# Kernel optimization log

Measured on AMD Instinct MI355X. Metric: run time of the kernel, lower is better.

The kernel has to match this reference:

```python
import jax, jax.numpy as jnp
from jax import lax
import numpy as np

R_ICO = 6          # resolution exponent r
CIN, COUT = 64, 64
RIN, ROUT = 6, 6
CHARTS = 5
H, W = 2 ** R_ICO, 2 ** (R_ICO + 1)
BATCH = 4


def _build_reorder_idx(r, R):
    H_, W_ = 2 ** r, 2 ** (r + 1)
    p = 2 ** r
    idx_in = np.arange(R * 5 * H_ * W_, dtype=np.int64).reshape(R, 5, H_, W_)
    out = np.zeros((R, 5, H_ + 2, W_ + 2), dtype=np.int64)
    out[..., 1:-1, 1:-1] = idx_in
    out[..., 0, 1:p + 1] = np.roll(idx_in, 1, -3)[..., -1, p:]
    out[..., 0, p + 1:-1] = np.roll(np.roll(idx_in, 1, -3), -1, -4)[..., :, -1][..., ::-1]
    out[..., -1, 2:p + 2] = np.roll(np.roll(idx_in, -1, -3), -1, -4)[..., :, 0][..., ::-1]
    out[..., -1, p + 1:-1] = np.roll(idx_in, -1, -3)[..., 0, 0:p]
    out[..., 1:-1, 0] = np.roll(np.roll(idx_in, 1, -3), 1, -4)[..., -1, 0:p][..., ::-1]
    out[..., 2:, -1] = np.roll(np.roll(idx_in, -1, -3), 1, -4)[..., 0, p:][..., ::-1]
    return out


_REORDER = jnp.asarray(_build_reorder_idx(R_ICO, RIN))

# 'baseline' hexagonal kernel index table (idx_k2 == idx_k for baseline)
_IDX_K = np.array([
    [5, 4, -1, 6, 0, 3, -1, 1, 2],
    [4, 3, -1, 5, 0, 2, -1, 6, 1],
    [3, 2, -1, 4, 0, 1, -1, 5, 6],
    [2, 1, -1, 3, 0, 6, -1, 4, 5],
    [1, 6, -1, 2, 0, 5, -1, 3, 4],
    [6, 5, -1, 1, 0, 4, -1, 2, 3]], dtype=np.int64) % 7
# per-output-rotation roll of the Rin axis: idx_r = arange(Rin) rolled i times
_RIN_MAP = np.stack([np.roll(np.arange(RIN), i) for i in range(ROUT)])  # (Rout, Rin)
_MASK3 = np.ones((3, 3), dtype=np.float32)
_MASK3[0, 2] = 0.0  # ret[..., 0, 2] = 0
_MASK3[2, 0] = 0.0  # ret[..., 2, 0] = 0

# CleanVertices: zero the two pole vertices of each chart
_VMASK = np.ones((H, W), dtype=np.float32)
_VMASK[0, -1] = 0.0
_VMASK[-1, 0] = 0.0


def _expand_kernel(weight):
    # weight: (Cout, Cin, Rin, 7)
    # K[co, ci, i, rj, k] = weight[co, ci, rin_map[i, rj], idx_k[i, k]]
    K = weight[:, :, _RIN_MAP[:, :, None], _IDX_K[:, None, :]]  # (Cout, Cin, Rout, Rin, 9)
    K = K.transpose(0, 2, 1, 3, 4).reshape(COUT, ROUT, CIN, RIN, 3, 3)
    K = K * _MASK3  # zero hex-grid corner taps
    # kernel_type='baseline' => idx_k2 == idx_k, so 0.5*K + 0.5*K2 == K
    return K.reshape(COUT * ROUT, CIN * RIN, 3, 3)


def setup_inputs() -> dict:
    key = jax.random.key(0)
    kx, kw = jax.random.split(key)
    s = float(np.sqrt(2.0 / (3 * 3 * CIN * RIN)))
    x = jax.random.normal(kx, (BATCH, CIN, RIN, CHARTS, H, W), dtype=jnp.float32)
    weight = s * jax.random.normal(kw, (COUT, CIN, RIN, 7), dtype=jnp.float32)
    bias = jnp.zeros((COUT,), dtype=jnp.float32)
    return {"x": x, "weight": weight, "bias": bias}


def reference(x, weight, bias):
    B = x.shape[0]
    # CleanVertices on input (inside PadIco.process_vertices)
    x = x * _VMASK
    # icosahedral gather padding: [B, C, R, 5, H, W] -> [B, C, R, 5, H+2, W+2]
    xf = x.reshape(B, CIN, -1)
    xp = jnp.take(xf, _REORDER, axis=-1)
    # fold (C R) -> channels and (charts, H+2) -> height
    ximg = xp.reshape(B, CIN * RIN, CHARTS * (H + 2), W + 2)
    kernel = _expand_kernel(weight)
    y = lax.conv_general_dilated(ximg, kernel, (1, 1), ((1, 1), (1, 1)),
                                 dimension_numbers=('NCHW', 'OIHW', 'NCHW'))
    y = y + jnp.repeat(bias, ROUT)[None, :, None, None]
    y = y.reshape(B, COUT, ROUT, CHARTS, H + 2, W + 2)[..., 1:-1, 1:-1]
    # CleanVertices on output
    return y * _VMASK
```

## Files before the change

### kernel.cpp

```cpp
#include <hip/hip_runtime.h>
#include <hip/hip_bf16.h>

#define BB    4
#define CIN_  64
#define RIN_  6
#define CH_   5
#define HH    64
#define WW_   128
#define KD    384
#define MD    384
#define PH    66
#define PW    130
#define PSZ   (PH*PW)

#define NTAP 7
#define WEXP2_ELEMS (NTAP*MD*KD)
#define WEXP2_BYTES (WEXP2_ELEMS*2)
#define NBORD 388

typedef __hip_bfloat16 bf16;
typedef __attribute__((ext_vector_type(8))) short bf16x8;
typedef __attribute__((ext_vector_type(4))) float f32x4;

__device__ const int TMAP[NTAP] = {0,1,3,4,5,7,8};
__device__ const int IDXK[6][9] = {
    {5,4,6,6,0,3,6,1,2},
    {4,3,6,5,0,2,6,6,1},
    {3,2,6,4,0,1,6,5,6},
    {2,1,6,3,0,6,6,4,5},
    {1,6,6,2,0,5,6,3,4},
    {6,5,6,1,0,4,6,2,3},
};

__global__ void wexp2_kernel(const float* __restrict__ w, bf16* __restrict__ W2) {
    int e = blockIdx.x * blockDim.x + threadIdx.x;
    if (e >= WEXP2_ELEMS) return;
    int k  = e % KD;
    int m  = (e / KD) % MD;
    int tt = e / (KD * MD);
    int t  = TMAP[tt];
    int co = m / 6, ro = m % 6, ci = k / 6, ri = k % 6;
    int rw = (ri - ro + 6) % 6;
    int s  = IDXK[ro][t];
    W2[e] = __float2bfloat16(w[((co * CIN_ + ci) * RIN_ + rw) * 7 + s]);
}

__global__ __launch_bounds__(256) void pad_interior(const float* __restrict__ x,
                                                    bf16* __restrict__ P) {
    int bid  = blockIdx.x;
    int kblk = bid % 3;
    int xh   = (bid / 3) & 1;
    int y    = (bid / 6) % 64;
    int bc   = bid / 384;
    int c = bc % 5, b = bc / 5;

    int lane = threadIdx.x & 63;
    int wv   = threadIdx.x >> 6;
    int k0   = kblk * 128 + wv * 32;
    int sx   = xh * 64 + lane;
    int xx   = sx + 1;

    bool mask0 = (y == 0 && sx == 127) || (y == 63 && sx == 0);

    const float* src = x + ((((size_t)(b * 384 + k0) * 5 + c) * 64 + y) * 128 + sx);
    unsigned int hbuf[16];
    #pragma unroll
    for (int kk = 0; kk < 32; kk += 2) {
        float v1 = src[(size_t)kk * 40960];
        float v2 = src[(size_t)(kk + 1) * 40960];
        if (mask0) { v1 = 0.f; v2 = 0.f; }
        bf16 h1 = __float2bfloat16(v1);
        bf16 h2 = __float2bfloat16(v2);
        hbuf[kk >> 1] = ((unsigned int)*(unsigned short*)&h2 << 16) |
                        (unsigned int)*(unsigned short*)&h1;
    }
    bf16* dst = P + (((size_t)(b * 5 + c) * PH + (y + 1)) * PW + xx) * KD + k0;
    uint4* d4 = (uint4*)dst;
    #pragma unroll
    for (int q = 0; q < 4; ++q)
        d4[q] = make_uint4(hbuf[4*q], hbuf[4*q+1], hbuf[4*q+2], hbuf[4*q+3]);
}

__global__ void pad_border(const float* __restrict__ x, bf16* __restrict__ P) {
    int e = blockIdx.x * blockDim.x + threadIdx.x;
    if (e >= 20 * NBORD * KD) return;
    int k  = e % KD;
    int p  = (e / KD) % NBORD;
    int bc = e / (KD * NBORD);
    int c = bc % 5, b = bc / 5;
    int yy, xx;
    if (p < 130)      { yy = 0;  xx = p; }
    else if (p < 260) { yy = 65; xx = p - 130; }
    else if (p < 324) { yy = 1 + (p - 260); xx = 0; }
    else              { yy = 1 + (p - 324); xx = 129; }

    int ci = k / RIN_, r = k % RIN_;
    int sr = r, sc = c, sy = 0, sx = 0;
    bool zi = false;
    if (xx == 129) {
        if (yy >= 2) { sr = (r + 5) % 6; sc = (c + 1) % 5; sy = 0; sx = 129 - yy; }
        else zi = true;
    } else if (yy == 0) {
        if (xx >= 1 && xx <= 64)        { sc = (c + 4) % 5; sy = 63; sx = 63 + xx; }
        else if (xx >= 65 && xx <= 128) { sr = (r + 1) % 6; sc = (c + 4) % 5; sy = 128 - xx; sx = 127; }
        else zi = true;
    } else if (yy == 65) {
        if (xx >= 65 && xx <= 128)      { sc = (c + 1) % 5; sy = 0; sx = xx - 65; }
        else if (xx >= 2 && xx <= 64)   { sr = (r + 1) % 6; sc = (c + 1) % 5; sy = 65 - xx; sx = 0; }
        else zi = true;
    } else {
        sr = (r + 5) % 6; sc = (c + 4) % 5; sy = 63; sx = 64 - yy;
    }
    if (zi) { sr = 0; sc = 0; sy = 0; sx = 0; }
    float v = x[((((size_t)b * 384 + (ci * 6 + sr)) * 5 + sc) * 64 + sy) * 128 + sx];
    if ((sy == 0 && sx == 127) || (sy == 63 && sx == 0)) v = 0.f;
    P[(((size_t)(b * 5 + c) * PH + yy) * PW + xx) * KD + k] = __float2bfloat16(v);
}

#define DYP 0x2950
#define DXP 0x2644

#define GLD(g, l) __builtin_amdgcn_global_load_lds( \
    (const __attribute__((address_space(1))) void*)(g), \
    (__attribute__((address_space(3))) void*)(l), 16, 0, 0)
#define MFMA_(a, b, c) __builtin_amdgcn_mfma_f32_16x16x32_bf16((a), (b), (c), 0, 0, 0)

__global__ __launch_bounds__(512) void conv_mfma8(
        const bf16* __restrict__ P, const bf16* __restrict__ W2,
        const float* __restrict__ bias, float* __restrict__ out) {
    __shared__ __align__(16) bf16 As[3][4096];
    __shared__ __align__(16) bf16 Bs[3][8192];

    const int bid = blockIdx.x;
    const int w   = (bid & 7) * 240 + (bid >> 3);
    const int mblk  = w % 3;
    const int ntile = (w / 3) % 32;
    const int bc    = w / 96;
    const int c = bc % 5, b = bc / 5;
    const int y0 = ntile * 2;

    const int tid  = threadIdx.x;
    const int lane = tid & 63;
    const int wv   = tid >> 6;
    const int wm   = wv >> 2, wn = wv & 3;
    const int lm   = lane & 15, lg = lane >> 4;

    const bf16* Pslice = P + (size_t)(b * 5 + c) * PSZ * KD;

    const int rA  = tid >> 2;
    const int kg  = (tid & 3) ^ ((rA >> 1) & 3);
    const bf16* gA0 = W2 + (size_t)(mblk * 128 + rA) * KD + kg * 8;
    const bf16* gB0 = Pslice + (size_t)rA * KD + kg * 8;

    int oA[4], oB[4];
    #pragma unroll
    for (int i = 0; i < 4; ++i) {
        int mm = wm * 64 + i * 16 + lm;
        oA[i] = (mm * 4 + (lg ^ ((mm >> 1) & 3))) * 16;
        int nn = wn * 64 + i * 16 + lm;
        oB[i] = (nn * 4 + (lg ^ ((nn >> 1) & 3))) * 16;
    }
    const char* Ab = (const char*)&As[0][0];
    const char* Bb = (const char*)&Bs[0][0];

    f32x4 acc[4][4] = {};

    #pragma unroll
    for (int t = 0; t < 2; ++t) {
        const bf16* ga = gA0 + t * 32;
        const bf16* gb = gB0 + (size_t)y0 * PW * KD + t * 32;
        GLD(ga, &As[t][wv * 512]);
        GLD(gb, &Bs[t][wv * 512]);
        GLD(gb + (size_t)PW * KD, &Bs[t][4096 + wv * 512]);
    }
    asm volatile("s_waitcnt vmcnt(3)" ::: "memory");
    __builtin_amdgcn_s_barrier();

    #pragma unroll 1
    for (int tt = 0; tt < 7; ++tt) {
        #pragma unroll
        for (int kc = 0; kc < 12; ++kc) {
            const int rb   = kc % 3;
            const int sb   = (kc + 2) % 3;
            const int skc  = (kc + 2) % 12;
            const int stt  = tt + (kc + 2) / 12;
            const bool dostage = (stt < 7);

            bf16x8 a0 = *(const bf16x8*)(Ab + rb * 8192 + oA[0]);
            bf16x8 a1 = *(const bf16x8*)(Ab + rb * 8192 + oA[1]);
            bf16x8 a2 = *(const bf16x8*)(Ab + rb * 8192 + oA[2]);
            bf16x8 a3 = *(const bf16x8*)(Ab + rb * 8192 + oA[3]);
            bf16x8 b0 = *(const bf16x8*)(Bb + rb * 16384 + oB[0]);
            bf16x8 b1 = *(const bf16x8*)(Bb + rb * 16384 + oB[1]);

            const bf16* gb = nullptr;
            if (dostage) {
                const int dy = (DYP >> (2 * stt)) & 3;
                const int dx = (DXP >> (2 * stt)) & 3;
                const bf16* ga = gA0 + (size_t)stt * (MD * KD) + skc * 32;
                gb = gB0 + ((size_t)(y0 + dy) * PW + dx) * KD + skc * 32;
                GLD(ga, &As[sb][wv * 512]);
                GLD(gb, &Bs[sb][wv * 512]);
            }
            __builtin_amdgcn_s_barrier();
            asm volatile("s_waitcnt lgkmcnt(0)" ::: "memory");
            __builtin_amdgcn_s_setprio(1);
            acc[0][0] = MFMA_(a0, b0, acc[0][0]);
            acc[1][0] = MFMA_(a1, b0, acc[1][0]);
            acc[2][0] = MFMA_(a2, b0, acc[2][0]);
            acc[3][0] = MFMA_(a3, b0, acc[3][0]);
            acc[0][1] = MFMA_(a0, b1, acc[0][1]);
            acc[1][1] = MFMA_(a1, b1, acc[1][1]);
            acc[2][1] = MFMA_(a2, b1, acc[2][1]);
            acc[3][1] = MFMA_(a3, b1, acc[3][1]);
            __builtin_amdgcn_s_setprio(0);
            __builtin_amdgcn_s_barrier();

            bf16x8 b2 = *(const bf16x8*)(Bb + rb * 16384 + oB[2]);
            bf16x8 b3 = *(const bf16x8*)(Bb + rb * 16384 + oB[3]);
            if (dostage) GLD(gb + (size_t)PW * KD, &Bs[sb][4096 + wv * 512]);
            __builtin_amdgcn_s_barrier();
            asm volatile("s_waitcnt lgkmcnt(0)" ::: "memory");
            __builtin_amdgcn_s_setprio(1);
            acc[0][2] = MFMA_(a0, b2, acc[0][2]);
            acc[1][2] = MFMA_(a1, b2, acc[1][2]);
            acc[2][2] = MFMA_(a2, b2, acc[2][2]);
            acc[3][2] = MFMA_(a3, b2, acc[3][2]);
            acc[0][3] = MFMA_(a0, b3, acc[0][3]);
            acc[1][3] = MFMA_(a1, b3, acc[1][3]);
            acc[2][3] = MFMA_(a2, b3, acc[2][3]);
            acc[3][3] = MFMA_(a3, b3, acc[3][3]);
            __builtin_amdgcn_s_setprio(0);
            if (tt == 6 && kc >= 10) {
                asm volatile("s_waitcnt vmcnt(0)" ::: "memory");
            } else {
                asm volatile("s_waitcnt vmcnt(3)" ::: "memory");
            }
            __builtin_amdgcn_s_barrier();
        }
    }

    const int m0 = mblk * 128 + wm * 64;
    const int yq = y0 + (wn >> 1);
    const int xb = (wn & 1) * 64;
    #pragma unroll
    for (int i = 0; i < 4; ++i) {
        #pragma unroll
        for (int r = 0; r < 4; ++r) {
            int m = m0 + i * 16 + lg * 4 + r;
            float bv = bias[m / 6];
            #pragma unroll
            for (int j = 0; j < 4; ++j) {
                int xq = xb + j * 16 + lm;
                float v = acc[i][j][r] + bv;
                if ((yq == 0 && xq == 127) || (yq == 63 && xq == 0)) v = 0.f;
                out[((size_t)(b * MD + m) * CH_ + c) * (HH * WW_) + yq * WW_ + xq] = v;
            }
        }
    }
}

extern "C" void kernel_launch(void* const* d_in, const int* in_sizes, int n_in,
                              void* d_out, int out_size, void* d_ws, size_t ws_size,
                              hipStream_t stream) {
    const float* x    = (const float*)d_in[0];
    const float* w    = (const float*)d_in[1];
    const float* bias = (const float*)d_in[2];
    float* out        = (float*)d_out;

    bf16* W2 = (bf16*)d_ws;
    bf16* P  = (bf16*)((char*)d_ws + WEXP2_BYTES);

    wexp2_kernel<<<(WEXP2_ELEMS + 255) / 256, 256, 0, stream>>>(w, W2);
    pad_interior<<<20 * 64 * 2 * 3, 256, 0, stream>>>(x, P);
    pad_border<<<(20 * NBORD * KD + 255) / 256, 256, 0, stream>>>(x, P);

    conv_mfma8<<<1920, 512, 0, stream>>>(P, W2, bias, out);
}
```

Measured before the change: 578.9 us.

## Use 4-wave blocks with 128x64 per-wave tiles in conv kernel

Changes the conv GEMM block from 8 waves (64x64 per wave) to 4 waves, each computing a 128x64 output tile with 8x4 accumulators. Each wave now issues more global-to-LDS loads per stage, and the vmcnt waits are adjusted to match. The aim is more MFMA work per LDS fragment read and fewer barriers per FLOP, with launch bounds allowing two blocks per CU. In exchange, accumulator and A-fragment registers double, which may hurt occupancy or cause spills.

Measured after the change: 507.4 us. 12.3% less time.

```diff
diff --git a/kernel.cpp b/kernel.cpp
--- a/kernel.cpp
+++ b/kernel.cpp
@@ -125,7 +125,7 @@
     (__attribute__((address_space(3))) void*)(l), 16, 0, 0)
 #define MFMA_(a, b, c) __builtin_amdgcn_mfma_f32_16x16x32_bf16((a), (b), (c), 0, 0, 0)
 
-__global__ __launch_bounds__(512) void conv_mfma8(
+__global__ __launch_bounds__(256, 2) void conv_mfma4(
         const bf16* __restrict__ P, const bf16* __restrict__ W2,
         const float* __restrict__ bias, float* __restrict__ out) {
     __shared__ __align__(16) bf16 As[3][4096];
@@ -142,38 +142,53 @@
     const int tid  = threadIdx.x;
     const int lane = tid & 63;
     const int wv   = tid >> 6;
-    const int wm   = wv >> 2, wn = wv & 3;
     const int lm   = lane & 15, lg = lane >> 4;
 
     const bf16* Pslice = P + (size_t)(b * 5 + c) * PSZ * KD;
 
-    const int rA  = tid >> 2;
-    const int kg  = (tid & 3) ^ ((rA >> 1) & 3);
-    const bf16* gA0 = W2 + (size_t)(mblk * 128 + rA) * KD + kg * 8;
-    const bf16* gB0 = Pslice + (size_t)rA * KD + kg * 8;
-
-    int oA[4], oB[4];
-    #pragma unroll
-    for (int i = 0; i < 4; ++i) {
-        int mm = wm * 64 + i * 16 + lm;
+    int oA[8], oB[4];
+    #pragma unroll
+    for (int i = 0; i < 8; ++i) {
+        int mm = i * 16 + lm;
         oA[i] = (mm * 4 + (lg ^ ((mm >> 1) & 3))) * 16;
-        int nn = wn * 64 + i * 16 + lm;
-        oB[i] = (nn * 4 + (lg ^ ((nn >> 1) & 3))) * 16;
+    }
+    #pragma unroll
+    for (int j = 0; j < 4; ++j) {
+        int nn = wv * 64 + j * 16 + lm;
+        oB[j] = (nn * 4 + (lg ^ ((nn >> 1) & 3))) * 16;
     }
     const char* Ab = (const char*)&As[0][0];
     const char* Bb = (const char*)&Bs[0][0];
 
-    f32x4 acc[4][4] = {};
+    const bf16* gA[2];
+    #pragma unroll
+    for (int q = 0; q < 2; ++q) {
+        int s = wv * 128 + q * 64 + lane;
+        int row = s >> 2, j = s & 3;
+        gA[q] = W2 + (size_t)(mblk * 128 + row) * KD + ((j ^ ((row >> 1) & 3)) << 3);
+    }
+    const bf16* gB[4];
+    #pragma unroll
+    for (int q = 0; q < 4; ++q) {
+        int s = wv * 256 + q * 64 + lane;
+        int col = s >> 2, j = s & 3;
+        int ncol = (col & 127) + (col >> 7) * PW;
+        gB[q] = Pslice + (size_t)ncol * KD + ((j ^ ((col >> 1) & 3)) << 3);
+    }
+
+    f32x4 acc[8][4] = {};
 
     #pragma unroll
     for (int t = 0; t < 2; ++t) {
-        const bf16* ga = gA0 + t * 32;
-        const bf16* gb = gB0 + (size_t)y0 * PW * KD + t * 32;
-        GLD(ga, &As[t][wv * 512]);
-        GLD(gb, &Bs[t][wv * 512]);
-        GLD(gb + (size_t)PW * KD, &Bs[t][4096 + wv * 512]);
-    }
-    asm volatile("s_waitcnt vmcnt(3)" ::: "memory");
+        size_t offA = (size_t)t * 32;
+        size_t offB = (size_t)y0 * PW * KD + t * 32;
+        GLD(gA[0] + offA, &As[t][(wv * 128) * 8]);
+        GLD(gA[1] + offA, &As[t][(wv * 128 + 64) * 8]);
+        #pragma unroll
+        for (int q = 0; q < 4; ++q)
+            GLD(gB[q] + offB, &Bs[t][(wv * 256 + q * 64) * 8]);
+    }
+    asm volatile("s_waitcnt vmcnt(6)" ::: "memory");
     __builtin_amdgcn_s_barrier();
 
     #pragma unroll 1
@@ -190,17 +205,23 @@
             bf16x8 a1 = *(const bf16x8*)(Ab + rb * 8192 + oA[1]);
             bf16x8 a2 = *(const bf16x8*)(Ab + rb * 8192 + oA[2]);
             bf16x8 a3 = *(const bf16x8*)(Ab + rb * 8192 + oA[3]);
+            bf16x8 a4 = *(const bf16x8*)(Ab + rb * 8192 + oA[4]);
+            bf16x8 a5 = *(const bf16x8*)(Ab + rb * 8192 + oA[5]);
+            bf16x8 a6 = *(const bf16x8*)(Ab + rb * 8192 + oA[6]);
+            bf16x8 a7 = *(const bf16x8*)(Ab + rb * 8192 + oA[7]);
             bf16x8 b0 = *(const bf16x8*)(Bb + rb * 16384 + oB[0]);
             bf16x8 b1 = *(const bf16x8*)(Bb + rb * 16384 + oB[1]);
 
-            const bf16* gb = nullptr;
+            size_t offA = 0, offB = 0;
             if (dostage) {
                 const int dy = (DYP >> (2 * stt)) & 3;
                 const int dx = (DXP >> (2 * stt)) & 3;
-                const bf16* ga = gA0 + (size_t)stt * (MD * KD) + skc * 32;
-                gb = gB0 + ((size_t)(y0 + dy) * PW + dx) * KD + skc * 32;
-                GLD(ga, &As[sb][wv * 512]);
-                GLD(gb, &Bs[sb][wv * 512]);
+                offA = (size_t)stt * (MD * KD) + skc * 32;
+                offB = ((size_t)(y0 + dy) * PW + dx) * KD + skc * 32;
+                GLD(gA[0] + offA, &As[sb][(wv * 128) * 8]);
+                GLD(gA[1] + offA, &As[sb][(wv * 128 + 64) * 8]);
+                GLD(gB[0] + offB, &Bs[sb][(wv * 256) * 8]);
+                GLD(gB[1] + offB, &Bs[sb][(wv * 256 + 64) * 8]);
             }
             __builtin_amdgcn_s_barrier();
             asm volatile("s_waitcnt lgkmcnt(0)" ::: "memory");
@@ -209,16 +230,27 @@
             acc[1][0] = MFMA_(a1, b0, acc[1][0]);
             acc[2][0] = MFMA_(a2, b0, acc[2][0]);
             acc[3][0] = MFMA_(a3, b0, acc[3][0]);
+            acc[4][0] = MFMA_(a4, b0, acc[4][0]);
+            acc[5][0] = MFMA_(a5, b0, acc[5][0]);
+            acc[6][0] = MFMA_(a6, b0, acc[6][0]);
+            acc[7][0] = MFMA_(a7, b0, acc[7][0]);
             acc[0][1] = MFMA_(a0, b1, acc[0][1]);
             acc[1][1] = MFMA_(a1, b1, acc[1][1]);
             acc[2][1] = MFMA_(a2, b1, acc[2][1]);
             acc[3][1] = MFMA_(a3, b1, acc[3][1]);
+            acc[4][1] = MFMA_(a4, b1, acc[4][1]);
+            acc[5][1] = MFMA_(a5, b1, acc[5][1]);
+            acc[6][1] = MFMA_(a6, b1, acc[6][1]);
+            acc[7][1] = MFMA_(a7, b1, acc[7][1]);
             __builtin_amdgcn_s_setprio(0);
             __builtin_amdgcn_s_barrier();
 
             bf16x8 b2 = *(const bf16x8*)(Bb + rb * 16384 + oB[2]);
             bf16x8 b3 = *(const bf16x8*)(Bb + rb * 16384 + oB[3]);
-            if (dostage) GLD(gb + (size_t)PW * KD, &Bs[sb][4096 + wv * 512]);
+            if (dostage) {
+                GLD(gB[2] + offB, &Bs[sb][(wv * 256 + 128) * 8]);
+                GLD(gB[3] + offB, &Bs[sb][(wv * 256 + 192) * 8]);
+            }
             __builtin_amdgcn_s_barrier();
             asm volatile("s_waitcnt lgkmcnt(0)" ::: "memory");
             __builtin_amdgcn_s_setprio(1);
@@ -226,25 +258,33 @@
             acc[1][2] = MFMA_(a1, b2, acc[1][2]);
             acc[2][2] = MFMA_(a2, b2, acc[2][2]);
             acc[3][2] = MFMA_(a3, b2, acc[3][2]);
+            acc[4][2] = MFMA_(a4, b2, acc[4][2]);
+            acc[5][2] = MFMA_(a5, b2, acc[5][2]);
+            acc[6][2] = MFMA_(a6, b2, acc[6][2]);
+            acc[7][2] = MFMA_(a7, b2, acc[7][2]);
             acc[0][3] = MFMA_(a0, b3, acc[0][3]);
             acc[1][3] = MFMA_(a1, b3, acc[1][3]);
             acc[2][3] = MFMA_(a2, b3, acc[2][3]);
             acc[3][3] = MFMA_(a3, b3, acc[3][3]);
+            acc[4][3] = MFMA_(a4, b3, acc[4][3]);
+            acc[5][3] = MFMA_(a5, b3, acc[5][3]);
+            acc[6][3] = MFMA_(a6, b3, acc[6][3]);
+            acc[7][3] = MFMA_(a7, b3, acc[7][3]);
             __builtin_amdgcn_s_setprio(0);
             if (tt == 6 && kc >= 10) {
                 asm volatile("s_waitcnt vmcnt(0)" ::: "memory");
             } else {
-                asm volatile("s_waitcnt vmcnt(3)" ::: "memory");
+                asm volatile("s_waitcnt vmcnt(6)" ::: "memory");
             }
             __builtin_amdgcn_s_barrier();
         }
     }
 
-    const int m0 = mblk * 128 + wm * 64;
-    const int yq = y0 + (wn >> 1);
-    const int xb = (wn & 1) * 64;
-    #pragma unroll
-    for (int i = 0; i < 4; ++i) {
+    const int m0 = mblk * 128;
+    const int yq = y0 + (wv >> 1);
+    const int xb = (wv & 1) * 64;
+    #pragma unroll
+    for (int i = 0; i < 8; ++i) {
         #pragma unroll
         for (int r = 0; r < 4; ++r) {
             int m = m0 + i * 16 + lg * 4 + r;
@@ -275,5 +315,5 @@
     pad_interior<<<20 * 64 * 2 * 3, 256, 0, stream>>>(x, P);
     pad_border<<<(20 * NBORD * KD + 255) / 256, 256, 0, stream>>>(x, P);
 
-    conv_mfma8<<<1920, 512, 0, stream>>>(P, W2, bias, out);
-}
+    conv_mfma4<<<1920, 256, 0, stream>>>(P, W2, bias, out);
+}
```

## Enlarge conv output tile to 128x512 per block, four image rows

Applied to the files above, without the earlier changes.

The MFMA conv kernel now computes four output rows (N=512) per block instead of two, with each wave holding a 64x128 accumulator tile. The grid shrinks from 1920 to 960 blocks. The aim is to reuse each weight tile across twice as many columns, halving weight traffic per output and cutting barriers per MFMA. In exchange it doubles accumulator registers and B-tile LDS (about 120 KB total), which may lower occupancy or cause spills. The smaller grid may also leave the tail of the schedule less evenly balanced.

Measured after the change: 537.7 us. -7.1%, faster.

```diff
diff --git a/kernel.cpp b/kernel.cpp
--- a/kernel.cpp
+++ b/kernel.cpp
@@ -125,55 +125,70 @@
     (__attribute__((address_space(3))) void*)(l), 16, 0, 0)
 #define MFMA_(a, b, c) __builtin_amdgcn_mfma_f32_16x16x32_bf16((a), (b), (c), 0, 0, 0)
 
-__global__ __launch_bounds__(512) void conv_mfma8(
+__global__ __launch_bounds__(512, 2) void conv_mfma8p(
         const bf16* __restrict__ P, const bf16* __restrict__ W2,
         const float* __restrict__ bias, float* __restrict__ out) {
     __shared__ __align__(16) bf16 As[3][4096];
-    __shared__ __align__(16) bf16 Bs[3][8192];
+    __shared__ __align__(16) bf16 Bs[3][16384];
 
     const int bid = blockIdx.x;
-    const int w   = (bid & 7) * 240 + (bid >> 3);
+    const int w   = (bid & 7) * 120 + (bid >> 3);
     const int mblk  = w % 3;
-    const int ntile = (w / 3) % 32;
-    const int bc    = w / 96;
+    const int ntile = (w / 3) % 16;
+    const int bc    = w / 48;
     const int c = bc % 5, b = bc / 5;
-    const int y0 = ntile * 2;
+    const int y0 = ntile * 4;
 
     const int tid  = threadIdx.x;
     const int lane = tid & 63;
     const int wv   = tid >> 6;
-    const int wm   = wv >> 2, wn = wv & 3;
+    const int mh   = wv >> 2;
+    const int nq   = wv & 3;
     const int lm   = lane & 15, lg = lane >> 4;
 
     const bf16* Pslice = P + (size_t)(b * 5 + c) * PSZ * KD;
 
-    const int rA  = tid >> 2;
-    const int kg  = (tid & 3) ^ ((rA >> 1) & 3);
-    const bf16* gA0 = W2 + (size_t)(mblk * 128 + rA) * KD + kg * 8;
-    const bf16* gB0 = Pslice + (size_t)rA * KD + kg * 8;
-
-    int oA[4], oB[4];
+    int oA[4], oB[8];
     #pragma unroll
     for (int i = 0; i < 4; ++i) {
-        int mm = wm * 64 + i * 16 + lm;
+        int mm = mh * 64 + i * 16 + lm;
         oA[i] = (mm * 4 + (lg ^ ((mm >> 1) & 3))) * 16;
-        int nn = wn * 64 + i * 16 + lm;
-        oB[i] = (nn * 4 + (lg ^ ((nn >> 1) & 3))) * 16;
+    }
+    #pragma unroll
+    for (int j = 0; j < 8; ++j) {
+        int nn = nq * 128 + j * 16 + lm;
+        oB[j] = (nn * 4 + (lg ^ ((nn >> 1) & 3))) * 16;
     }
     const char* Ab = (const char*)&As[0][0];
     const char* Bb = (const char*)&Bs[0][0];
 
-    f32x4 acc[4][4] = {};
+    const bf16* gA;
+    {
+        int s = tid;
+        int row = s >> 2, j = s & 3;
+        gA = W2 + (size_t)(mblk * 128 + row) * KD + ((j ^ ((row >> 1) & 3)) << 3);
+    }
+    const bf16* gB[4];
+    #pragma unroll
+    for (int q = 0; q < 4; ++q) {
+        int s = q * 512 + tid;
+        int col = s >> 2, j = s & 3;
+        int ncol = (col & 127) + (col >> 7) * PW;
+        gB[q] = Pslice + (size_t)ncol * KD + ((j ^ ((col >> 1) & 3)) << 3);
+    }
+
+    f32x4 acc[4][8] = {};
 
     #pragma unroll
     for (int t = 0; t < 2; ++t) {
-        const bf16* ga = gA0 + t * 32;
-        const bf16* gb = gB0 + (size_t)y0 * PW * KD + t * 32;
-        GLD(ga, &As[t][wv * 512]);
-        GLD(gb, &Bs[t][wv * 512]);
-        GLD(gb + (size_t)PW * KD, &Bs[t][4096 + wv * 512]);
-    }
-    asm volatile("s_waitcnt vmcnt(3)" ::: "memory");
+        size_t offA = (size_t)t * 32;
+        size_t offB = (size_t)y0 * PW * KD + t * 32;
+        GLD(gA + offA, &As[t][(wv * 64) * 8]);
+        #pragma unroll
+        for (int q = 0; q < 4; ++q)
+            GLD(gB[q] + offB, &Bs[t][(q * 512 + wv * 64) * 8]);
+    }
+    asm volatile("s_waitcnt vmcnt(5)" ::: "memory");
     __builtin_amdgcn_s_barrier();
 
     #pragma unroll 1
@@ -185,22 +200,28 @@
             const int skc  = (kc + 2) % 12;
             const int stt  = tt + (kc + 2) / 12;
             const bool dostage = (stt < 7);
+            const bool drain   = (tt == 6 && kc >= 10);
+
+            size_t offA = 0, offB = 0;
+            if (dostage) {
+                const int dy = (DYP >> (2 * stt)) & 3;
+                const int dx = (DXP >> (2 * stt)) & 3;
+                offA = (size_t)stt * (MD * KD) + skc * 32;
+                offB = ((size_t)(y0 + dy) * PW + dx) * KD + skc * 32;
+            }
 
             bf16x8 a0 = *(const bf16x8*)(Ab + rb * 8192 + oA[0]);
             bf16x8 a1 = *(const bf16x8*)(Ab + rb * 8192 + oA[1]);
             bf16x8 a2 = *(const bf16x8*)(Ab + rb * 8192 + oA[2]);
             bf16x8 a3 = *(const bf16x8*)(Ab + rb * 8192 + oA[3]);
-            bf16x8 b0 = *(const bf16x8*)(Bb + rb * 16384 + oB[0]);
-            bf16x8 b1 = *(const bf16x8*)(Bb + rb * 16384 + oB[1]);
-
-            const bf16* gb = nullptr;
+            bf16x8 b0 = *(const bf16x8*)(Bb + rb * 32768 + oB[0]);
+            bf16x8 b1 = *(const bf16x8*)(Bb + rb * 32768 + oB[1]);
+            bf16x8 b2 = *(const bf16x8*)(Bb + rb * 32768 + oB[2]);
+            bf16x8 b3 = *(const bf16x8*)(Bb + rb * 32768 + oB[3]);
             if (dostage) {
-                const int dy = (DYP >> (2 * stt)) & 3;
-                const int dx = (DXP >> (2 * stt)) & 3;
-                const bf16* ga = gA0 + (size_t)stt * (MD * KD) + skc * 32;
-                gb = gB0 + ((size_t)(y0 + dy) * PW + dx) * KD + skc * 32;
-                GLD(ga, &As[sb][wv * 512]);
-                GLD(gb, &Bs[sb][wv * 512]);
+                GLD(gA + offA, &As[sb][(wv * 64) * 8]);
+                GLD(gB[0] + offB, &Bs[sb][(0 * 512 + wv * 64) * 8]);
+                GLD(gB[1] + offB, &Bs[sb][(1 * 512 + wv * 64) * 8]);
             }
             __builtin_amdgcn_s_barrier();
             asm volatile("s_waitcnt lgkmcnt(0)" ::: "memory");
@@ -213,15 +234,6 @@
             acc[1][1] = MFMA_(a1, b1, acc[1][1]);
             acc[2][1] = MFMA_(a2, b1, acc[2][1]);
             acc[3][1] = MFMA_(a3, b1, acc[3][1]);
-            __builtin_amdgcn_s_setprio(0);
-            __builtin_amdgcn_s_barrier();
-
-            bf16x8 b2 = *(const bf16x8*)(Bb + rb * 16384 + oB[2]);
-            bf16x8 b3 = *(const bf16x8*)(Bb + rb * 16384 + oB[3]);
-            if (dostage) GLD(gb + (size_t)PW * KD, &Bs[sb][4096 + wv * 512]);
-            __builtin_amdgcn_s_barrier();
-            asm volatile("s_waitcnt lgkmcnt(0)" ::: "memory");
-            __builtin_amdgcn_s_setprio(1);
             acc[0][2] = MFMA_(a0, b2, acc[0][2]);
             acc[1][2] = MFMA_(a1, b2, acc[1][2]);
             acc[2][2] = MFMA_(a2, b2, acc[2][2]);
@@ -231,18 +243,47 @@
             acc[2][3] = MFMA_(a2, b3, acc[2][3]);
             acc[3][3] = MFMA_(a3, b3, acc[3][3]);
             __builtin_amdgcn_s_setprio(0);
-            if (tt == 6 && kc >= 10) {
+            __builtin_amdgcn_s_barrier();
+
+            bf16x8 b4 = *(const bf16x8*)(Bb + rb * 32768 + oB[4]);
+            bf16x8 b5 = *(const bf16x8*)(Bb + rb * 32768 + oB[5]);
+            bf16x8 b6 = *(const bf16x8*)(Bb + rb * 32768 + oB[6]);
+            bf16x8 b7 = *(const bf16x8*)(Bb + rb * 32768 + oB[7]);
+            if (dostage) {
+                GLD(gB[2] + offB, &Bs[sb][(2 * 512 + wv * 64) * 8]);
+                GLD(gB[3] + offB, &Bs[sb][(3 * 512 + wv * 64) * 8]);
+            }
+            __builtin_amdgcn_s_barrier();
+            asm volatile("s_waitcnt lgkmcnt(0)" ::: "memory");
+            __builtin_amdgcn_s_setprio(1);
+            acc[0][4] = MFMA_(a0, b4, acc[0][4]);
+            acc[1][4] = MFMA_(a1, b4, acc[1][4]);
+            acc[2][4] = MFMA_(a2, b4, acc[2][4]);
+            acc[3][4] = MFMA_(a3, b4, acc[3][4]);
+            acc[0][5] = MFMA_(a0, b5, acc[0][5]);
+            acc[1][5] = MFMA_(a1, b5, acc[1][5]);
+            acc[2][5] = MFMA_(a2, b5, acc[2][5]);
+            acc[3][5] = MFMA_(a3, b5, acc[3][5]);
+            acc[0][6] = MFMA_(a0, b6, acc[0][6]);
+            acc[1][6] = MFMA_(a1, b6, acc[1][6]);
+            acc[2][6] = MFMA_(a2, b6, acc[2][6]);
+            acc[3][6] = MFMA_(a3, b6, acc[3][6]);
+            acc[0][7] = MFMA_(a0, b7, acc[0][7]);
+            acc[1][7] = MFMA_(a1, b7, acc[1][7]);
+            acc[2][7] = MFMA_(a2, b7, acc[2][7]);
+            acc[3][7] = MFMA_(a3, b7, acc[3][7]);
+            __builtin_amdgcn_s_setprio(0);
+            if (drain) {
                 asm volatile("s_waitcnt vmcnt(0)" ::: "memory");
             } else {
-                asm volatile("s_waitcnt vmcnt(3)" ::: "memory");
+                asm volatile("s_waitcnt vmcnt(5)" ::: "memory");
             }
             __builtin_amdgcn_s_barrier();
         }
     }
 
-    const int m0 = mblk * 128 + wm * 64;
-    const int yq = y0 + (wn >> 1);
-    const int xb = (wn & 1) * 64;
+    const int m0 = mblk * 128 + mh * 64;
+    const int yq = y0 + nq;
     #pragma unroll
     for (int i = 0; i < 4; ++i) {
         #pragma unroll
@@ -250,8 +291,8 @@
             int m = m0 + i * 16 + lg * 4 + r;
             float bv = bias[m / 6];
             #pragma unroll
-            for (int j = 0; j < 4; ++j) {
-                int xq = xb + j * 16 + lm;
+            for (int j = 0; j < 8; ++j) {
+                int xq = j * 16 + lm;
                 float v = acc[i][j][r] + bv;
                 if ((yq == 0 && xq == 127) || (yq == 63 && xq == 0)) v = 0.f;
                 out[((size_t)(b * MD + m) * CH_ + c) * (HH * WW_) + yq * WW_ + xq] = v;
@@ -275,5 +316,5 @@
     pad_interior<<<20 * 64 * 2 * 3, 256, 0, stream>>>(x, P);
     pad_border<<<(20 * NBORD * KD + 255) / 256, 256, 0, stream>>>(x, P);
 
-    conv_mfma8<<<1920, 512, 0, stream>>>(P, W2, bias, out);
-}
+    conv_mfma8p<<<960, 512, 0, stream>>>(P, W2, bias, out);
+}
```

## Stage 4-row input strip once per k-chunk and reuse it across all seven taps

Applied to the files above, without the earlier changes.

Replaces the per-tap staging of shifted input tiles with a single LDS strip of four padded rows per 32-wide k-chunk. Each of the seven hex taps then reads from this strip at a dy/dx offset, so input global traffic drops by roughly the tap count. Weights are now loaded straight from global into registers with double buffering, and the block shrinks to 256 threads with 8x4 accumulators per wave and two blocks per CU. This cuts LDS staging and barriers per MFMA, at the cost of higher register pressure and weight fragments that are no longer shared through LDS.

New measurement: 1.284 ms. 2.22x slower.

```diff
diff --git a/kernel.cpp b/kernel.cpp
--- a/kernel.cpp
+++ b/kernel.cpp
@@ -117,19 +117,73 @@
     P[(((size_t)(b * 5 + c) * PH + yy) * PW + xx) * KD + k] = __float2bfloat16(v);
 }
 
-#define DYP 0x2950
-#define DXP 0x2644
-
 #define GLD(g, l) __builtin_amdgcn_global_load_lds( \
     (const __attribute__((address_space(1))) void*)(g), \
     (__attribute__((address_space(3))) void*)(l), 16, 0, 0)
 #define MFMA_(a, b, c) __builtin_amdgcn_mfma_f32_16x16x32_bf16((a), (b), (c), 0, 0, 0)
 
-__global__ __launch_bounds__(512) void conv_mfma8(
+#define BODY(KC, J, DYv, DXv, SB, AC, AN, LAST_IT) {                              \
+    if (!(LAST_IT)) {        \
+        const int ntt = ((J) + 1) % 7;                                            \
+        const int nkc = (KC) + ((J) + 1) / 7;                                     \
+        const bf16* ap = gAbase + (size_t)ntt * (MD * KD) + nkc * 32;             \
+        AN[0] = *(const bf16x8*)(ap + 0 * (16 * KD));                             \
+        AN[1] = *(const bf16x8*)(ap + 1 * (16 * KD));                             \
+        AN[2] = *(const bf16x8*)(ap + 2 * (16 * KD));                             \
+        AN[3] = *(const bf16x8*)(ap + 3 * (16 * KD));                             \
+        AN[4] = *(const bf16x8*)(ap + 4 * (16 * KD));                             \
+        AN[5] = *(const bf16x8*)(ap + 5 * (16 * KD));                             \
+        AN[6] = *(const bf16x8*)(ap + 6 * (16 * KD));                             \
+        AN[7] = *(const bf16x8*)(ap + 7 * (16 * KD));                             \
+    }                                                                             \
+    if ((J) == 0 && (KC) < 11) {    \
+        const int ko = ((KC) + 1) * 64;                                           \
+        GLD(Pbyte + so[0] + ko, &Ss[((KC) + 1) & 1][(wv * 528 + 0 * 64) * 8]);    \
+        GLD(Pbyte + so[1] + ko, &Ss[((KC) + 1) & 1][(wv * 528 + 1 * 64) * 8]);    \
+        GLD(Pbyte + so[2] + ko, &Ss[((KC) + 1) & 1][(wv * 528 + 2 * 64) * 8]);    \
+        GLD(Pbyte + so[3] + ko, &Ss[((KC) + 1) & 1][(wv * 528 + 3 * 64) * 8]);    \
+        GLD(Pbyte + so[4] + ko, &Ss[((KC) + 1) & 1][(wv * 528 + 4 * 64) * 8]);    \
+        GLD(Pbyte + so[5] + ko, &Ss[((KC) + 1) & 1][(wv * 528 + 5 * 64) * 8]);    \
+        GLD(Pbyte + so[6] + ko, &Ss[((KC) + 1) & 1][(wv * 528 + 6 * 64) * 8]);    \
+        GLD(Pbyte + so[7] + ko, &Ss[((KC) + 1) & 1][(wv * 528 + 7 * 64) * 8]);    \
+        GLD(Pbyte + so[8] + ko, &Ss[((KC) + 1) & 1][(wv * 528 + 8 * 64) * 8]);    \
+    }                                                                             \
+    {                                           \
+        const char* sbase = (const char*)&Ss[SB][0] + (rrw + (DYv)) * 8448;       \
+        bf16x8 bv0 = *(const bf16x8*)(sbase + oBt[DXv][0]);                       \
+        bf16x8 bv1 = *(const bf16x8*)(sbase + oBt[DXv][1]);                       \
+        bf16x8 bv2 = *(const bf16x8*)(sbase + oBt[DXv][2]);                       \
+        bf16x8 bv3 = *(const bf16x8*)(sbase + oBt[DXv][3]);                       \
+        __builtin_amdgcn_s_setprio(1);                                            \
+        acc[0][0]=MFMA_(AC[0],bv0,acc[0][0]); acc[1][0]=MFMA_(AC[1],bv0,acc[1][0]);\
+        acc[2][0]=MFMA_(AC[2],bv0,acc[2][0]); acc[3][0]=MFMA_(AC[3],bv0,acc[3][0]);\
+        acc[4][0]=MFMA_(AC[4],bv0,acc[4][0]); acc[5][0]=MFMA_(AC[5],bv0,acc[5][0]);\
+        acc[6][0]=MFMA_(AC[6],bv0,acc[6][0]); acc[7][0]=MFMA_(AC[7],bv0,acc[7][0]);\
+        acc[0][1]=MFMA_(AC[0],bv1,acc[0][1]); acc[1][1]=MFMA_(AC[1],bv1,acc[1][1]);\
+        acc[2][1]=MFMA_(AC[2],bv1,acc[2][1]); acc[3][1]=MFMA_(AC[3],bv1,acc[3][1]);\
+        acc[4][1]=MFMA_(AC[4],bv1,acc[4][1]); acc[5][1]=MFMA_(AC[5],bv1,acc[5][1]);\
+        acc[6][1]=MFMA_(AC[6],bv1,acc[6][1]); acc[7][1]=MFMA_(AC[7],bv1,acc[7][1]);\
+        acc[0][2]=MFMA_(AC[0],bv2,acc[0][2]); acc[1][2]=MFMA_(AC[1],bv2,acc[1][2]);\
+        acc[2][2]=MFMA_(AC[2],bv2,acc[2][2]); acc[3][2]=MFMA_(AC[3],bv2,acc[3][2]);\
+        acc[4][2]=MFMA_(AC[4],bv2,acc[4][2]); acc[5][2]=MFMA_(AC[5],bv2,acc[5][2]);\
+        acc[6][2]=MFMA_(AC[6],bv2,acc[6][2]); acc[7][2]=MFMA_(AC[7],bv2,acc[7][2]);\
+        acc[0][3]=MFMA_(AC[0],bv3,acc[0][3]); acc[1][3]=MFMA_(AC[1],bv3,acc[1][3]);\
+        acc[2][3]=MFMA_(AC[2],bv3,acc[2][3]); acc[3][3]=MFMA_(AC[3],bv3,acc[3][3]);\
+        acc[4][3]=MFMA_(AC[4],bv3,acc[4][3]); acc[5][3]=MFMA_(AC[5],bv3,acc[5][3]);\
+        acc[6][3]=MFMA_(AC[6],bv3,acc[6][3]); acc[7][3]=MFMA_(AC[7],bv3,acc[7][3]);\
+        __builtin_amdgcn_s_setprio(0);                                            \
+    }                                                                             \
+    if ((J) == 6 && !(LAST_IT)) {                                                 \
+            \
+        asm volatile("s_waitcnt vmcnt(8)" ::: "memory");                          \
+        __builtin_amdgcn_s_barrier();                                             \
+    }                                                                             \
+}
+
+__global__ __launch_bounds__(256, 2) void conv_strip(
         const bf16* __restrict__ P, const bf16* __restrict__ W2,
         const float* __restrict__ bias, float* __restrict__ out) {
-    __shared__ __align__(16) bf16 As[3][4096];
-    __shared__ __align__(16) bf16 Bs[3][8192];
+    __shared__ __align__(16) bf16 Ss[2][17280];
 
     const int bid = blockIdx.x;
     const int w   = (bid & 7) * 240 + (bid >> 3);
@@ -142,109 +196,72 @@
     const int tid  = threadIdx.x;
     const int lane = tid & 63;
     const int wv   = tid >> 6;
-    const int wm   = wv >> 2, wn = wv & 3;
     const int lm   = lane & 15, lg = lane >> 4;
+    const int rrw  = wv >> 1;
 
     const bf16* Pslice = P + (size_t)(b * 5 + c) * PSZ * KD;
-
-    const int rA  = tid >> 2;
-    const int kg  = (tid & 3) ^ ((rA >> 1) & 3);
-    const bf16* gA0 = W2 + (size_t)(mblk * 128 + rA) * KD + kg * 8;
-    const bf16* gB0 = Pslice + (size_t)rA * KD + kg * 8;
-
-    int oA[4], oB[4];
-    #pragma unroll
-    for (int i = 0; i < 4; ++i) {
-        int mm = wm * 64 + i * 16 + lm;
-        oA[i] = (mm * 4 + (lg ^ ((mm >> 1) & 3))) * 16;
-        int nn = wn * 64 + i * 16 + lm;
-        oB[i] = (nn * 4 + (lg ^ ((nn >> 1) & 3))) * 16;
-    }
-    const char* Ab = (const char*)&As[0][0];
-    const char* Bb = (const char*)&Bs[0][0];
-
-    f32x4 acc[4][4] = {};
-
-    #pragma unroll
-    for (int t = 0; t < 2; ++t) {
-        const bf16* ga = gA0 + t * 32;
-        const bf16* gb = gB0 + (size_t)y0 * PW * KD + t * 32;
-        GLD(ga, &As[t][wv * 512]);
-        GLD(gb, &Bs[t][wv * 512]);
-        GLD(gb + (size_t)PW * KD, &Bs[t][4096 + wv * 512]);
-    }
-    asm volatile("s_waitcnt vmcnt(3)" ::: "memory");
+    const char* Pbyte  = (const char*)Pslice;
+
+    const bf16* gAbase = W2 + (size_t)(mblk * 128 + lm) * KD + 8 * lg;
+
+    unsigned so[9];
+    #pragma unroll
+    for (int r9 = 0; r9 < 9; ++r9) {
+        int s  = wv * 528 + r9 * 64 + lane;
+        int r  = (s / 528) & 3;
+        int cc = (s % 528) >> 2;
+        if (cc >= 130) cc &= 127;
+        int kg = s & 3;
+        so[r9] = (unsigned)((((y0 + r) * PW + cc) * KD + 8 * (kg ^ ((cc >> 1) & 3))) * 2);
+    }
+
+    int oBt[3][4];
+    #pragma unroll
+    for (int dx = 0; dx < 3; ++dx)
+        #pragma unroll
+        for (int j4 = 0; j4 < 4; ++j4) {
+            int cc = dx + (wv & 1) * 64 + j4 * 16 + lm;
+            oBt[dx][j4] = (cc * 4 + (lg ^ ((cc >> 1) & 3))) * 16;
+        }
+
+    f32x4 acc[8][4] = {};
+    bf16x8 aA[8], aB[8];
+
+    #pragma unroll
+    for (int r9 = 0; r9 < 9; ++r9)
+        GLD(Pbyte + so[r9], &Ss[0][(wv * 528 + r9 * 64) * 8]);
+    #pragma unroll
+    for (int i = 0; i < 8; ++i)
+        aA[i] = *(const bf16x8*)(gAbase + (size_t)i * (16 * KD));
+    asm volatile("s_waitcnt vmcnt(8)" ::: "memory");
     __builtin_amdgcn_s_barrier();
 
     #pragma unroll 1
-    for (int tt = 0; tt < 7; ++tt) {
-        #pragma unroll
-        for (int kc = 0; kc < 12; ++kc) {
-            const int rb   = kc % 3;
-            const int sb   = (kc + 2) % 3;
-            const int skc  = (kc + 2) % 12;
-            const int stt  = tt + (kc + 2) / 12;
-            const bool dostage = (stt < 7);
-
-            bf16x8 a0 = *(const bf16x8*)(Ab + rb * 8192 + oA[0]);
-            bf16x8 a1 = *(const bf16x8*)(Ab + rb * 8192 + oA[1]);
-            bf16x8 a2 = *(const bf16x8*)(Ab + rb * 8192 + oA[2]);
-            bf16x8 a3 = *(const bf16x8*)(Ab + rb * 8192 + oA[3]);
-            bf16x8 b0 = *(const bf16x8*)(Bb + rb * 16384 + oB[0]);
-            bf16x8 b1 = *(const bf16x8*)(Bb + rb * 16384 + oB[1]);
-
-            const bf16* gb = nullptr;
-            if (dostage) {
-                const int dy = (DYP >> (2 * stt)) & 3;
-                const int dx = (DXP >> (2 * stt)) & 3;
-                const bf16* ga = gA0 + (size_t)stt * (MD * KD) + skc * 32;
-                gb = gB0 + ((size_t)(y0 + dy) * PW + dx) * KD + skc * 32;
-                GLD(ga, &As[sb][wv * 512]);
-                GLD(gb, &Bs[sb][wv * 512]);
-            }
-            __builtin_amdgcn_s_barrier();
-            asm volatile("s_waitcnt lgkmcnt(0)" ::: "memory");
-            __builtin_amdgcn_s_setprio(1);
-            acc[0][0] = MFMA_(a0, b0, acc[0][0]);
-            acc[1][0] = MFMA_(a1, b0, acc[1][0]);
-            acc[2][0] = MFMA_(a2, b0, acc[2][0]);
-            acc[3][0] = MFMA_(a3, b0, acc[3][0]);
-            acc[0][1] = MFMA_(a0, b1, acc[0][1]);
-            acc[1][1] = MFMA_(a1, b1, acc[1][1]);
-            acc[2][1] = MFMA_(a2, b1, acc[2][1]);
-            acc[3][1] = MFMA_(a3, b1, acc[3][1]);
-            __builtin_amdgcn_s_setprio(0);
-            __builtin_amdgcn_s_barrier();
-
-            bf16x8 b2 = *(const bf16x8*)(Bb + rb * 16384 + oB[2]);
-            bf16x8 b3 = *(const bf16x8*)(Bb + rb * 16384 + oB[3]);
-            if (dostage) GLD(gb + (size_t)PW * KD, &Bs[sb][4096 + wv * 512]);
-            __builtin_amdgcn_s_barrier();
-            asm volatile("s_waitcnt lgkmcnt(0)" ::: "memory");
-            __builtin_amdgcn_s_setprio(1);
-            acc[0][2] = MFMA_(a0, b2, acc[0][2]);
-            acc[1][2] = MFMA_(a1, b2, acc[1][2]);
-            acc[2][2] = MFMA_(a2, b2, acc[2][2]);
-            acc[3][2] = MFMA_(a3, b2, acc[3][2]);
-            acc[0][3] = MFMA_(a0, b3, acc[0][3]);
-            acc[1][3] = MFMA_(a1, b3, acc[1][3]);
-            acc[2][3] = MFMA_(a2, b3, acc[2][3]);
-            acc[3][3] = MFMA_(a3, b3, acc[3][3]);
-            __builtin_amdgcn_s_setprio(0);
-            if (tt == 6 && kc >= 10) {
-                asm volatile("s_waitcnt vmcnt(0)" ::: "memory");
-            } else {
-                asm volatile("s_waitcnt vmcnt(3)" ::: "memory");
-            }
-            __builtin_amdgcn_s_barrier();
-        }
-    }
-
-    const int m0 = mblk * 128 + wm * 64;
-    const int yq = y0 + (wn >> 1);
-    const int xb = (wn & 1) * 64;
-    #pragma unroll
-    for (int i = 0; i < 4; ++i) {
+    for (int kc2 = 0; kc2 < 6; ++kc2) {
+        const int kcA = kc2 * 2;
+        const int kcB = kcA + 1;
+        const bool last = (kc2 == 5);
+        BODY(kcA, 0, 0, 0, 0, aA, aB, false)
+        BODY(kcA, 1, 0, 1, 0, aB, aA, false)
+        BODY(kcA, 2, 1, 0, 0, aA, aB, false)
+        BODY(kcA, 3, 1, 1, 0, aB, aA, false)
+        BODY(kcA, 4, 1, 2, 0, aA, aB, false)
+        BODY(kcA, 5, 2, 1, 0, aB, aA, false)
+        BODY(kcA, 6, 2, 2, 0, aA, aB, false)
+        BODY(kcB, 0, 0, 0, 1, aB, aA, false)
+        BODY(kcB, 1, 0, 1, 1, aA, aB, false)
+        BODY(kcB, 2, 1, 0, 1, aB, aA, false)
+        BODY(kcB, 3, 1, 1, 1, aA, aB, false)
+        BODY(kcB, 4, 1, 2, 1, aB, aA, false)
+        BODY(kcB, 5, 2, 1, 1, aA, aB, false)
+        BODY(kcB, 6, 2, 2, 1, aB, aA, last)
+    }
+
+    const int m0 = mblk * 128;
+    const int yq = y0 + rrw;
+    const int xb = (wv & 1) * 64;
+    #pragma unroll
+    for (int i = 0; i < 8; ++i) {
         #pragma unroll
         for (int r = 0; r < 4; ++r) {
             int m = m0 + i * 16 + lg * 4 + r;
@@ -275,5 +292,5 @@
     pad_interior<<<20 * 64 * 2 * 3, 256, 0, stream>>>(x, P);
     pad_border<<<(20 * NBORD * KD + 255) / 256, 256, 0, stream>>>(x, P);
 
-    conv_mfma8<<<1920, 512, 0, stream>>>(P, W2, bias, out);
-}
+    conv_strip<<<1920, 256, 0, stream>>>(P, W2, bias, out);
+}
```
